# Optimization experiments

Hardware: AMD Instinct MI355X
Metric: run time of the kernel (lower is better)

Reference implementation:

```python
import jax, jax.numpy as jnp
import numpy as np

N_HEAD = 50000
N_TAIL = 50000
E = 800000
F_IN = 256
D = 64
H = 4
FE = 64
N_ETYPES = 5
NEG_SLOPE = 0.2


def setup_inputs() -> dict:
    key = jax.random.key(0)
    ks = jax.random.split(key, 10)
    head_feature = jax.random.normal(ks[0], (N_HEAD, F_IN), jnp.float32)
    tail_feature = jax.random.normal(ks[1], (N_TAIL, F_IN), jnp.float32)
    head_ind = jax.random.randint(ks[2], (E,), 0, N_HEAD)
    tail_ind = jax.random.randint(ks[3], (E,), 0, N_TAIL)
    edge_list = jnp.stack([head_ind, tail_ind], axis=0)  # [2, E]
    tmp_edge = jax.random.randint(ks[4], (E,), 0, N_ETYPES)
    s = 0.05  # small init scale, mimics uniform(-stdv, stdv)
    W = jax.random.normal(ks[5], (F_IN, D * H), jnp.float32) * s
    W_e = jax.random.normal(ks[6], (FE, FE * H), jnp.float32) * s
    edge_emb = jax.random.normal(ks[7], (N_ETYPES, FE), jnp.float32) * s
    a_l = jax.random.normal(ks[8], (1, H, D), jnp.float32) * s
    a_r = jax.random.normal(jax.random.fold_in(ks[8], 1), (1, H, D), jnp.float32) * s
    a_e = jax.random.normal(ks[9], (1, H, FE), jnp.float32) * s
    return {
        "head_feature": head_feature,
        "tail_feature": tail_feature,
        "edge_list": edge_list,
        "tmp_edge": tmp_edge,
        "W": W,
        "W_e": W_e,
        "edge_emb": edge_emb,
        "a_l": a_l,
        "a_r": a_r,
        "a_e": a_e,
    }


def _layer(head_feature, tail_feature, head_ind, tail_ind, tmp_edge,
           W, W_e, edge_emb, a_l, a_r, a_e):
    n_head = head_feature.shape[0]
    # dense projections (dropout = identity in eval)
    h_head = (head_feature @ W).reshape(-1, H, D)      # [N_h, H, D]
    h_tail = (tail_feature @ W).reshape(-1, H, D)      # [N_t, H, D]
    e = (edge_emb @ W_e).reshape(-1, H, FE)            # [T, H, FE]
    # per-edge attention logits
    h_l = (a_l * h_head).sum(-1)[head_ind]             # [E, H]
    h_r = (a_r * h_tail).sum(-1)[tail_ind]             # [E, H]
    h_e = (a_e * e).sum(-1)[tmp_edge]                  # [E, H]
    score = jax.nn.leaky_relu(h_l + h_r + h_e, NEG_SLOPE)
    # segment softmax over edges grouped by destination (head) node, per head
    m = jax.ops.segment_max(score, head_ind, num_segments=n_head)   # [N_h, H]
    ex = jnp.exp(score - m[head_ind])                               # [E, H]
    z = jax.ops.segment_sum(ex, head_ind, num_segments=n_head)      # [N_h, H]
    alpha = ex / z[head_ind]                                        # [E, H]
    # weighted aggregation: sparse-mm per head, vectorized over heads
    msg = alpha[:, :, None] * h_tail[tail_ind]                      # [E, H, D]
    out = jax.ops.segment_sum(msg, head_ind, num_segments=n_head)   # [N_h, H, D]
    out = out.reshape(n_head, H * D)
    return jax.nn.elu(out)


def reference(head_feature, tail_feature, edge_list, tmp_edge,
              W, W_e, edge_emb, a_l, a_r, a_e):
    head_ind = edge_list[0]
    tail_ind = edge_list[1]
    return _layer(head_feature, tail_feature, head_ind, tail_ind, tmp_edge,
                  W, W_e, edge_emb, a_l, a_r, a_e)
```

## Files before the change

### kernel.cpp

```cpp
#include <hip/hip_runtime.h>
#include <hip/hip_bf16.h>
#include <math.h>

#define N_HEADN 50000
#define N_TAILN 50000
#define NE      800000
#define F_IN    256
#define HH      4
#define HD      256
#define FE      64
#define N_ETYPES 5
#define NEG_SLOPE 0.2f
#define NB_SCAN ((N_HEADN + 255) / 256)
#define NB_CVT  ((N_TAILN * F_IN) / (256 * 16))

typedef __attribute__((ext_vector_type(8))) short bf16x8;
typedef __attribute__((ext_vector_type(4))) float f32x4;

static __device__ __forceinline__ unsigned short f2bf(float f) {
    unsigned u = __float_as_uint(f);
    return (unsigned short)((u + 0x7FFF + ((u >> 16) & 1)) >> 16);
}
static __device__ __forceinline__ float bf2f(unsigned short u) {
    return __uint_as_float((unsigned)u << 16);
}

__global__ __launch_bounds__(256) void prep_kernel(const float* __restrict__ X,
                                                   unsigned short* __restrict__ Xb,
                                                   const float* __restrict__ W,
                                                   const float* __restrict__ a_l,
                                                   const float* __restrict__ W_e,
                                                   const float* __restrict__ a_e,
                                                   const float* __restrict__ edge_emb,
                                                   float* __restrict__ waT,
                                                   float* __restrict__ heo,
                                                   short* __restrict__ Wt) {
    const int b = blockIdx.x;
    if (b < NB_CVT) {
        size_t t = (size_t)b * 256 + threadIdx.x;
        const float4* xp = (const float4*)X + t * 4;
        float4 v0 = xp[0], v1 = xp[1], v2 = xp[2], v3 = xp[3];
        bf16x8 o0, o1;
        o0[0] = (short)f2bf(v0.x); o0[1] = (short)f2bf(v0.y);
        o0[2] = (short)f2bf(v0.z); o0[3] = (short)f2bf(v0.w);
        o0[4] = (short)f2bf(v1.x); o0[5] = (short)f2bf(v1.y);
        o0[6] = (short)f2bf(v1.z); o0[7] = (short)f2bf(v1.w);
        o1[0] = (short)f2bf(v2.x); o1[1] = (short)f2bf(v2.y);
        o1[2] = (short)f2bf(v2.z); o1[3] = (short)f2bf(v2.w);
        o1[4] = (short)f2bf(v3.x); o1[5] = (short)f2bf(v3.y);
        o1[6] = (short)f2bf(v3.z); o1[7] = (short)f2bf(v3.w);
        bf16x8* op = (bf16x8*)(Xb + t * 16);
        op[0] = o0;
        op[1] = o1;
    } else if (b == NB_CVT) {
        int k = threadIdx.x;
        #pragma unroll
        for (int h = 0; h < HH; ++h) {
            float s = 0.f;
            for (int d = 0; d < 64; ++d) s += a_l[h * 64 + d] * W[(size_t)k * HD + h * 64 + d];
            waT[h * 256 + k] = s;
        }
    } else if (b == NB_CVT + 1) {
        __shared__ float wae[FE][HH];
        int t = threadIdx.x;
        int k = t >> 2, h = t & 3;
        float s = 0.f;
        for (int f = 0; f < 64; ++f) s += a_e[h * 64 + f] * W_e[(size_t)k * (FE * HH) + h * 64 + f];
        wae[k][h] = s;
        __syncthreads();
        if (t < N_ETYPES * HH) {
            int ty = t >> 2, hh = t & 3;
            float acc = 0.f;
            for (int kk = 0; kk < FE; ++kk) acc += edge_emb[ty * FE + kk] * wae[kk][hh];
            heo[ty * HH + hh] = acc;
        }
    } else {
        int n = b - (NB_CVT + 2), k = threadIdx.x;
        Wt[(size_t)n * 256 + k] = (short)f2bf(W[(size_t)k * 256 + n]);
    }
}

__global__ void hist_kernel(const int* __restrict__ head, int* __restrict__ counts) {
    int e = blockIdx.x * 256 + threadIdx.x;
    atomicAdd(&counts[head[e]], 1);
}

__global__ void blocksum_kernel(const int* __restrict__ counts, int* __restrict__ blockSums) {
    __shared__ int s[256];
    int t = threadIdx.x, j = blockIdx.x * 256 + t;
    s[t] = (j < N_HEADN) ? counts[j] : 0;
    __syncthreads();
    for (int off = 128; off > 0; off >>= 1) {
        if (t < off) s[t] += s[t + off];
        __syncthreads();
    }
    if (t == 0) blockSums[blockIdx.x] = s[0];
}

__global__ void blockscan_kernel(const int* __restrict__ blockSums, int* __restrict__ blockOff) {
    __shared__ int s[256];
    int t = threadIdx.x;
    int v = (t < NB_SCAN) ? blockSums[t] : 0;
    s[t] = v;
    __syncthreads();
    for (int off = 1; off < 256; off <<= 1) {
        int u = (t >= off) ? s[t - off] : 0;
        __syncthreads();
        s[t] += u;
        __syncthreads();
    }
    if (t < NB_SCAN) blockOff[t] = s[t] - v;
}

__global__ void rowstart_kernel(const int* __restrict__ counts, const int* __restrict__ blockOff,
                                int* __restrict__ row_start, int* __restrict__ cursor) {
    __shared__ int s[256];
    int t = threadIdx.x, j = blockIdx.x * 256 + t;
    int c = (j < N_HEADN) ? counts[j] : 0;
    s[t] = c;
    __syncthreads();
    for (int off = 1; off < 256; off <<= 1) {
        int u = (t >= off) ? s[t - off] : 0;
        __syncthreads();
        s[t] += u;
        __syncthreads();
    }
    int excl = blockOff[blockIdx.x] + s[t] - c;
    if (j < N_HEADN) {
        row_start[j] = excl;
        cursor[j]    = excl;
        if (j == N_HEADN - 1) row_start[N_HEADN] = excl + c;
    }
}

__global__ __launch_bounds__(256) void head_dot_kernel(const float* __restrict__ X,
                                                       const float* __restrict__ waT,
                                                       float* __restrict__ hl) {
    const int wave = threadIdx.x >> 6;
    const int lane = threadIdx.x & 63;
    const int n = blockIdx.x * 4 + wave;
    float4 x = ((const float4*)(X + (size_t)n * F_IN))[lane];
    float p[HH];
    #pragma unroll
    for (int h = 0; h < HH; ++h) {
        float4 w = ((const float4*)(waT + h * 256))[lane];
        p[h] = x.x * w.x + x.y * w.y + x.z * w.z + x.w * w.w;
    }
    #pragma unroll
    for (int off = 1; off < 64; off <<= 1) {
        #pragma unroll
        for (int h = 0; h < HH; ++h) p[h] += __shfl_xor(p[h], off);
    }
    if (lane < HH) hl[(size_t)n * HH + lane] = p[lane];
}

__global__ __launch_bounds__(256) void proj_mfma_kernel(const unsigned short* __restrict__ Xb,
                                                        const short* __restrict__ Wt,
                                                        const float* __restrict__ a,
                                                        unsigned short* __restrict__ h_out,
                                                        float* __restrict__ dot_out,
                                                        int N) {
    const int tid  = threadIdx.x;
    const int w    = tid >> 6;
    const int lane = tid & 63;
    const int quad = lane >> 4;
    const int l15  = lane & 15;
    const int n0   = blockIdx.x * 32;

    const bool valid1 = (n0 + 16) < N;

    f32x4 acc[2][4];
    #pragma unroll
    for (int mt = 0; mt < 2; ++mt)
        #pragma unroll
        for (int ct = 0; ct < 4; ++ct)
            acc[mt][ct] = (f32x4){0.f, 0.f, 0.f, 0.f};

    const unsigned short* xbase0 = Xb + (size_t)(n0 + l15) * F_IN + quad * 8;
    const unsigned short* xbase1 = Xb + (size_t)(n0 + 16 + l15) * F_IN + quad * 8;
    const short* wbase  = Wt + (size_t)(w * 64 + l15) * 256 + quad * 8;

    #pragma unroll
    for (int k0 = 0; k0 < 256; k0 += 32) {
        bf16x8 a0 = *(const bf16x8*)(xbase0 + k0);
        bf16x8 a1;
        if (valid1) a1 = *(const bf16x8*)(xbase1 + k0);
        #pragma unroll
        for (int ct = 0; ct < 4; ++ct) {
            bf16x8 bfrag = *(const bf16x8*)(wbase + (size_t)ct * 16 * 256 + k0);
            acc[0][ct] = __builtin_amdgcn_mfma_f32_16x16x32_bf16(a0, bfrag, acc[0][ct], 0, 0, 0);
            if (valid1)
                acc[1][ct] = __builtin_amdgcn_mfma_f32_16x16x32_bf16(a1, bfrag, acc[1][ct], 0, 0, 0);
        }
    }

    float av[4];
    #pragma unroll
    for (int ct = 0; ct < 4; ++ct) av[ct] = a[w * 64 + ct * 16 + l15];

    #pragma unroll
    for (int mt = 0; mt < 2; ++mt) {
        if (mt == 1 && !valid1) break;
        #pragma unroll
        for (int ct = 0; ct < 4; ++ct) {
            #pragma unroll
            for (int r = 0; r < 4; ++r) {
                int row = n0 + mt * 16 + quad * 4 + r;
                h_out[(size_t)row * HD + w * 64 + ct * 16 + l15] = f2bf(acc[mt][ct][r]);
            }
        }
        #pragma unroll
        for (int r = 0; r < 4; ++r) {
            float p = av[0] * acc[mt][0][r] + av[1] * acc[mt][1][r]
                    + av[2] * acc[mt][2][r] + av[3] * acc[mt][3][r];
            p += __shfl_xor(p, 1);
            p += __shfl_xor(p, 2);
            p += __shfl_xor(p, 4);
            p += __shfl_xor(p, 8);
            if (l15 == 0) {
                int row = n0 + mt * 16 + quad * 4 + r;
                dot_out[(size_t)row * HH + w] = p;
            }
        }
    }
}

__global__ void scatter_kernel(const int* __restrict__ head, const int* __restrict__ tail,
                               const int* __restrict__ etype,
                               const float* __restrict__ hl, const float* __restrict__ hr,
                               const float* __restrict__ he,
                               int* __restrict__ cursor, int* __restrict__ packed,
                               float* __restrict__ exE) {
    int e = blockIdx.x * 256 + threadIdx.x;
    int h0 = head[e];
    int tl = tail[e];
    int ty = etype[e];
    float4 L = *(const float4*)(hl + (size_t)h0 * HH);
    float4 R = *(const float4*)(hr + (size_t)tl * HH);
    float4 T = *(const float4*)(he + ty * HH);
    float s0 = L.x + R.x + T.x;
    float s1 = L.y + R.y + T.y;
    float s2 = L.z + R.z + T.z;
    float s3 = L.w + R.w + T.w;
    s0 = (s0 > 0.f) ? s0 : NEG_SLOPE * s0;
    s1 = (s1 > 0.f) ? s1 : NEG_SLOPE * s1;
    s2 = (s2 > 0.f) ? s2 : NEG_SLOPE * s2;
    s3 = (s3 > 0.f) ? s3 : NEG_SLOPE * s3;
    float w0 = __expf(s0), w1 = __expf(s1), w2 = __expf(s2), w3 = __expf(s3);
    int pos = atomicAdd(&cursor[h0], 1);
    packed[pos] = tl;
    *(float4*)(exE + (size_t)pos * HH) = make_float4(w0, w1, w2, w3);
}

__global__ __launch_bounds__(256) void agg_kernel(const int* __restrict__ row_start,
                                                  const int* __restrict__ packed,
                                                  const float* __restrict__ exE,
                                                  const unsigned short* __restrict__ h_tail,
                                                  float* __restrict__ out) {
    const int wave = threadIdx.x >> 6;
    const int lane = threadIdx.x & 63;
    const int n = blockIdx.x * 4 + wave;
    const int s = row_start[n];
    const int e = row_start[n + 1];
    const int g = lane >> 4;
    const int q = lane & 15;
    const int h = q >> 2;

    float acc[16];
    #pragma unroll
    for (int c = 0; c < 16; ++c) acc[c] = 0.f;
    float z = 0.f;

    for (int i = s; i < e; i += 4) {
        const int ei = i + g;
        if (ei < e) {
            const int tl = packed[ei];
            const float w = exE[(size_t)ei * HH + h];
            const uint4* p = (const uint4*)(h_tail + (size_t)tl * HD + q * 16);
            uint4 u0 = p[0];
            uint4 u1 = p[1];
            #pragma unroll
            for (int j = 0; j < 4; ++j) {
                unsigned u = ((const unsigned*)&u0)[j];
                acc[2 * j]     += w * __uint_as_float(u << 16);
                acc[2 * j + 1] += w * __uint_as_float(u & 0xFFFF0000u);
            }
            #pragma unroll
            for (int j = 0; j < 4; ++j) {
                unsigned u = ((const unsigned*)&u1)[j];
                acc[8 + 2 * j]     += w * __uint_as_float(u << 16);
                acc[8 + 2 * j + 1] += w * __uint_as_float(u & 0xFFFF0000u);
            }
            z += w;
        }
    }

    #pragma unroll
    for (int c = 0; c < 16; ++c) {
        acc[c] += __shfl_xor(acc[c], 16);
        acc[c] += __shfl_xor(acc[c], 32);
    }
    z += __shfl_xor(z, 16);
    z += __shfl_xor(z, 32);

    float4 o;
    if (z > 0.f) {
        o.x = acc[g * 4 + 0] / z;
        o.y = acc[g * 4 + 1] / z;
        o.z = acc[g * 4 + 2] / z;
        o.w = acc[g * 4 + 3] / z;
        o.x = (o.x > 0.f) ? o.x : expm1f(o.x);
        o.y = (o.y > 0.f) ? o.y : expm1f(o.y);
        o.z = (o.z > 0.f) ? o.z : expm1f(o.z);
        o.w = (o.w > 0.f) ? o.w : expm1f(o.w);
    } else {
        o = make_float4(0.f, 0.f, 0.f, 0.f);
    }
    ((float4*)(out + (size_t)n * HD))[q * 4 + g] = o;
}

extern "C" void kernel_launch(void* const* d_in, const int* in_sizes, int n_in,
                              void* d_out, int out_size, void* d_ws, size_t ws_size,
                              hipStream_t stream) {
    const float* head_feature = (const float*)d_in[0];
    const float* tail_feature = (const float*)d_in[1];
    const int*   edge_list    = (const int*)d_in[2];
    const int*   tmp_edge     = (const int*)d_in[3];
    const float* W            = (const float*)d_in[4];
    const float* W_e          = (const float*)d_in[5];
    const float* edge_emb     = (const float*)d_in[6];
    const float* a_l          = (const float*)d_in[7];
    const float* a_r          = (const float*)d_in[8];
    const float* a_e          = (const float*)d_in[9];
    const int* head_ind = edge_list;
    const int* tail_ind = edge_list + NE;

    char* ws = (char*)d_ws;
    unsigned short* h_tail = (unsigned short*)ws; ws += sizeof(unsigned short) * (size_t)N_TAILN * HD;
    unsigned short* Xb = (unsigned short*)ws;
    float* exE    = (float*)(void*)Xb;
    int*   packed = (int*)(void*)((char*)(void*)Xb + sizeof(float) * (size_t)NE * HH);
    ws += sizeof(unsigned short) * (size_t)N_TAILN * HD;
    short* Wt        = (short*)ws; ws += sizeof(short) * 256 * 256;
    float* hl        = (float*)ws; ws += sizeof(float) * (size_t)N_HEADN * HH;
    float* hr        = (float*)ws; ws += sizeof(float) * (size_t)N_TAILN * HH;
    float* waT       = (float*)ws; ws += sizeof(float) * HH * 256;
    float* he        = (float*)ws; ws += sizeof(float) * 32;
    int*   counts    = (int*)ws;   ws += sizeof(int) * (size_t)N_HEADN;
    int*   row_start = (int*)ws;   ws += sizeof(int) * (size_t)(N_HEADN + 4);
    int*   cursor    = (int*)ws;   ws += sizeof(int) * (size_t)N_HEADN;
    int*   blockSums = (int*)ws;   ws += sizeof(int) * 256;
    int*   blockOff  = (int*)ws;   ws += sizeof(int) * 256;

    hipMemsetAsync(counts, 0, sizeof(int) * (size_t)N_HEADN, stream);

    hipLaunchKernelGGL(prep_kernel, dim3(NB_CVT + 258), dim3(256), 0, stream,
                       tail_feature, Xb, W, a_l, W_e, a_e, edge_emb, waT, he, Wt);

    hipLaunchKernelGGL(hist_kernel, dim3(NE / 256), dim3(256), 0, stream,
                       head_ind, counts);
    hipLaunchKernelGGL(blocksum_kernel, dim3(NB_SCAN), dim3(256), 0, stream,
                       counts, blockSums);
    hipLaunchKernelGGL(blockscan_kernel, dim3(1), dim3(256), 0, stream,
                       blockSums, blockOff);
    hipLaunchKernelGGL(rowstart_kernel, dim3(NB_SCAN), dim3(256), 0, stream,
                       counts, blockOff, row_start, cursor);

    hipLaunchKernelGGL(head_dot_kernel, dim3(N_HEADN / 4), dim3(256), 0, stream,
                       head_feature, waT, hl);
    hipLaunchKernelGGL(proj_mfma_kernel, dim3((N_TAILN + 31) / 32), dim3(256), 0, stream,
                       Xb, Wt, a_r, h_tail, hr, N_TAILN);

    hipLaunchKernelGGL(scatter_kernel, dim3(NE / 256), dim3(256), 0, stream,
                       head_ind, tail_ind, tmp_edge, hl, hr, he, cursor, packed, exE);

    hipLaunchKernelGGL(agg_kernel, dim3(N_HEADN / 4), dim3(256), 0, stream,
                       row_start, packed, exE, h_tail, (float*)d_out);
}
```

Baseline: 370.8 us.

## Fold counts memset into prep, widen projection tile, batch neighbor index loads

Three independent changes. The separate memset of the counts array is folded into extra blocks of the prep kernel, saving one launch. The MFMA projection kernel now computes 64 rows per block instead of 32, reusing each W fragment across four row tiles and clamping the last tile so the valid-row branch goes away. The aggregation kernel loads 64 neighbor indices per wave at once and broadcasts them with shuffles, instead of each lane group loading its own index per step. The costs are higher register pressure in the projection kernel and fewer blocks in its grid.

Result: faster. 360.2 us (-2.9%).

```diff
diff --git a/kernel.cpp b/kernel.cpp
--- a/kernel.cpp
+++ b/kernel.cpp
@@ -34,7 +34,8 @@
                                                    const float* __restrict__ edge_emb,
                                                    float* __restrict__ waT,
                                                    float* __restrict__ heo,
-                                                   short* __restrict__ Wt) {
+                                                   short* __restrict__ Wt,
+                                                   int* __restrict__ counts) {
     const int b = blockIdx.x;
     if (b < NB_CVT) {
         size_t t = (size_t)b * 256 + threadIdx.x;
@@ -74,9 +75,12 @@
             for (int kk = 0; kk < FE; ++kk) acc += edge_emb[ty * FE + kk] * wae[kk][hh];
             heo[ty * HH + hh] = acc;
         }
-    } else {
+    } else if (b < NB_CVT + 2 + 256) {
         int n = b - (NB_CVT + 2), k = threadIdx.x;
         Wt[(size_t)n * 256 + k] = (short)f2bf(W[(size_t)k * 256 + n]);
+    } else {
+        int j = (b - (NB_CVT + 258)) * 256 + threadIdx.x;
+        if (j < N_HEADN) counts[j] = 0;
     }
 }
 
@@ -165,32 +169,39 @@
     const int lane = tid & 63;
     const int quad = lane >> 4;
     const int l15  = lane & 15;
-    const int n0   = blockIdx.x * 32;
-
-    const bool valid1 = (n0 + 16) < N;
-
-    f32x4 acc[2][4];
-    #pragma unroll
-    for (int mt = 0; mt < 2; ++mt)
+    const int n0   = blockIdx.x * 64;
+
+    int rbase[4];
+    #pragma unroll
+    for (int mt = 0; mt < 4; ++mt) {
+        int r = n0 + mt * 16;
+        rbase[mt] = (r + 16 <= N) ? r : (N - 16);
+    }
+
+    f32x4 acc[4][4];
+    #pragma unroll
+    for (int mt = 0; mt < 4; ++mt)
         #pragma unroll
         for (int ct = 0; ct < 4; ++ct)
             acc[mt][ct] = (f32x4){0.f, 0.f, 0.f, 0.f};
 
-    const unsigned short* xbase0 = Xb + (size_t)(n0 + l15) * F_IN + quad * 8;
-    const unsigned short* xbase1 = Xb + (size_t)(n0 + 16 + l15) * F_IN + quad * 8;
-    const short* wbase  = Wt + (size_t)(w * 64 + l15) * 256 + quad * 8;
-
-    #pragma unroll
+    const short* wbase = Wt + (size_t)(w * 64 + l15) * 256 + quad * 8;
+    const unsigned short* xb[4];
+    #pragma unroll
+    for (int mt = 0; mt < 4; ++mt)
+        xb[mt] = Xb + (size_t)(rbase[mt] + l15) * F_IN + quad * 8;
+
+    #pragma unroll 2
     for (int k0 = 0; k0 < 256; k0 += 32) {
-        bf16x8 a0 = *(const bf16x8*)(xbase0 + k0);
-        bf16x8 a1;
-        if (valid1) a1 = *(const bf16x8*)(xbase1 + k0);
+        bf16x8 af[4];
+        #pragma unroll
+        for (int mt = 0; mt < 4; ++mt) af[mt] = *(const bf16x8*)(xb[mt] + k0);
         #pragma unroll
         for (int ct = 0; ct < 4; ++ct) {
             bf16x8 bfrag = *(const bf16x8*)(wbase + (size_t)ct * 16 * 256 + k0);
-            acc[0][ct] = __builtin_amdgcn_mfma_f32_16x16x32_bf16(a0, bfrag, acc[0][ct], 0, 0, 0);
-            if (valid1)
-                acc[1][ct] = __builtin_amdgcn_mfma_f32_16x16x32_bf16(a1, bfrag, acc[1][ct], 0, 0, 0);
+            #pragma unroll
+            for (int mt = 0; mt < 4; ++mt)
+                acc[mt][ct] = __builtin_amdgcn_mfma_f32_16x16x32_bf16(af[mt], bfrag, acc[mt][ct], 0, 0, 0);
         }
     }
 
@@ -199,13 +210,12 @@
     for (int ct = 0; ct < 4; ++ct) av[ct] = a[w * 64 + ct * 16 + l15];
 
     #pragma unroll
-    for (int mt = 0; mt < 2; ++mt) {
-        if (mt == 1 && !valid1) break;
+    for (int mt = 0; mt < 4; ++mt) {
         #pragma unroll
         for (int ct = 0; ct < 4; ++ct) {
             #pragma unroll
             for (int r = 0; r < 4; ++r) {
-                int row = n0 + mt * 16 + quad * 4 + r;
+                int row = rbase[mt] + quad * 4 + r;
                 h_out[(size_t)row * HD + w * 64 + ct * 16 + l15] = f2bf(acc[mt][ct][r]);
             }
         }
@@ -218,7 +228,7 @@
             p += __shfl_xor(p, 4);
             p += __shfl_xor(p, 8);
             if (l15 == 0) {
-                int row = n0 + mt * 16 + quad * 4 + r;
+                int row = rbase[mt] + quad * 4 + r;
                 dot_out[(size_t)row * HH + w] = p;
             }
         }
@@ -271,27 +281,33 @@
     for (int c = 0; c < 16; ++c) acc[c] = 0.f;
     float z = 0.f;
 
-    for (int i = s; i < e; i += 4) {
-        const int ei = i + g;
-        if (ei < e) {
-            const int tl = packed[ei];
-            const float w = exE[(size_t)ei * HH + h];
-            const uint4* p = (const uint4*)(h_tail + (size_t)tl * HD + q * 16);
-            uint4 u0 = p[0];
-            uint4 u1 = p[1];
-            #pragma unroll
-            for (int j = 0; j < 4; ++j) {
-                unsigned u = ((const unsigned*)&u0)[j];
-                acc[2 * j]     += w * __uint_as_float(u << 16);
-                acc[2 * j + 1] += w * __uint_as_float(u & 0xFFFF0000u);
+    for (int base = s; base < e; base += 64) {
+        const int cnt = (e - base < 64) ? (e - base) : 64;
+        int myidx = 0;
+        if (base + lane < e) myidx = packed[base + lane];
+        #pragma unroll 4
+        for (int i = 0; i < cnt; i += 4) {
+            const int j = i + g;
+            const int tl = __shfl(myidx, j);
+            if (j < cnt) {
+                const float w = exE[(size_t)(base + j) * HH + h];
+                const uint4* p = (const uint4*)(h_tail + (size_t)tl * HD + q * 16);
+                uint4 u0 = p[0];
+                uint4 u1 = p[1];
+                #pragma unroll
+                for (int jj = 0; jj < 4; ++jj) {
+                    unsigned u = ((const unsigned*)&u0)[jj];
+                    acc[2 * jj]     += w * __uint_as_float(u << 16);
+                    acc[2 * jj + 1] += w * __uint_as_float(u & 0xFFFF0000u);
+                }
+                #pragma unroll
+                for (int jj = 0; jj < 4; ++jj) {
+                    unsigned u = ((const unsigned*)&u1)[jj];
+                    acc[8 + 2 * jj]     += w * __uint_as_float(u << 16);
+                    acc[8 + 2 * jj + 1] += w * __uint_as_float(u & 0xFFFF0000u);
+                }
+                z += w;
             }
-            #pragma unroll
-            for (int j = 0; j < 4; ++j) {
-                unsigned u = ((const unsigned*)&u1)[j];
-                acc[8 + 2 * j]     += w * __uint_as_float(u << 16);
-                acc[8 + 2 * j + 1] += w * __uint_as_float(u & 0xFFFF0000u);
-            }
-            z += w;
         }
     }
 
@@ -352,10 +368,8 @@
     int*   blockSums = (int*)ws;   ws += sizeof(int) * 256;
     int*   blockOff  = (int*)ws;   ws += sizeof(int) * 256;
 
-    hipMemsetAsync(counts, 0, sizeof(int) * (size_t)N_HEADN, stream);
-
-    hipLaunchKernelGGL(prep_kernel, dim3(NB_CVT + 258), dim3(256), 0, stream,
-                       tail_feature, Xb, W, a_l, W_e, a_e, edge_emb, waT, he, Wt);
+    hipLaunchKernelGGL(prep_kernel, dim3(NB_CVT + 258 + NB_SCAN), dim3(256), 0, stream,
+                       tail_feature, Xb, W, a_l, W_e, a_e, edge_emb, waT, he, Wt, counts);
 
     hipLaunchKernelGGL(hist_kernel, dim3(NE / 256), dim3(256), 0, stream,
                        head_ind, counts);
@@ -368,7 +382,7 @@
 
     hipLaunchKernelGGL(head_dot_kernel, dim3(N_HEADN / 4), dim3(256), 0, stream,
                        head_feature, waT, hl);
-    hipLaunchKernelGGL(proj_mfma_kernel, dim3((N_TAILN + 31) / 32), dim3(256), 0, stream,
+    hipLaunchKernelGGL(proj_mfma_kernel, dim3((N_TAILN + 63) / 64), dim3(256), 0, stream,
                        Xb, Wt, a_r, h_tail, hr, N_TAILN);
 
     hipLaunchKernelGGL(scatter_kernel, dim3(NE / 256), dim3(256), 0, stream,
```
